# Kernel optimization log

Hardware: AMD Instinct MI355X
Metric: run time of the kernel (lower is better)

## Reference

```python
import jax, jax.numpy as jnp
import numpy as np

HIDDEN = 1024
FFN = 3584
N_EXPERTS = 8
TOP_K = 2


def setup_inputs() -> dict:
    key = jax.random.key(0)
    k1, k2, k3, k4 = jax.random.split(key, 4)
    B, S = 1, 1024
    hidden_states = jax.random.normal(k1, (B, S, HIDDEN), dtype=jnp.float32)
    gate_w = jax.random.normal(k2, (N_EXPERTS, HIDDEN), dtype=jnp.float32) * 0.02
    w_gate_up = jax.random.normal(k3, (N_EXPERTS, HIDDEN, 2 * FFN), dtype=jnp.float32) * 0.02
    w_down = jax.random.normal(k4, (N_EXPERTS, FFN, HIDDEN), dtype=jnp.float32) * 0.02
    return {"hidden_states": hidden_states, "gate_w": gate_w,
            "w_gate_up": w_gate_up, "w_down": w_down}


def reference(hidden_states, gate_w, w_gate_up, w_down):
    B, S, H = hidden_states.shape
    x = hidden_states.reshape(-1, H)                       # [T, H]
    T = x.shape[0]
    E = gate_w.shape[0]

    # Router
    router_logits = x @ gate_w.T                           # [T, E]
    probs = jax.nn.softmax(router_logits.astype(jnp.float32), axis=-1)
    routing_weights, selected = jax.lax.top_k(probs, TOP_K)  # [T, k]
    routing_weights = routing_weights / routing_weights.sum(-1, keepdims=True)

    # Dense combine matrix equivalent to permute->grouped GEMM->unpermute
    combine = jnp.zeros((T, E), probs.dtype).at[
        jnp.arange(T)[:, None], selected].add(routing_weights)  # [T, E]

    # Grouped SwiGLU expert MLPs (all experts over all tokens, masked by combine)
    gu = jnp.einsum('th,ehf->etf', x, w_gate_up)           # [E, T, 2F]
    Fdim = w_down.shape[1]
    gate_proj, up_proj = gu[..., :Fdim], gu[..., Fdim:]
    act = jax.nn.silu(gate_proj) * up_proj                 # [E, T, F]
    down = jnp.einsum('etf,efh->eth', act, w_down)         # [E, T, H]
    out = jnp.einsum('eth,te->th', down, combine.astype(down.dtype))
    return out.reshape(B, S, H), router_logits
```

## Files before the change

### kernel.cpp

```cpp
#include <hip/hip_runtime.h>
#include <hip/hip_bf16.h>
#include <math.h>

#define H 1024
#define F 3584
#define F2 7168
#define NE 8
#define T 1024

typedef __attribute__((ext_vector_type(4))) float f32x4;
typedef __attribute__((ext_vector_type(8))) short bf16x8;
typedef __attribute__((ext_vector_type(4))) unsigned u32x4;

__device__ inline short f2bf(float f) {
  union { float f; unsigned u; } v; v.f = f;
  unsigned r = (v.u + 0x7FFFu + ((v.u >> 16) & 1u)) >> 16;
  return (short)r;
}

__device__ inline unsigned pkbf(float a, float b) {
  unsigned r;
  asm("v_cvt_pk_bf16_f32 %0, %1, %2" : "=v"(r) : "v"(a), "v"(b));
  return r;
}

__device__ inline void gload16(const void* g, void* l) {
  __builtin_amdgcn_global_load_lds(
      (const __attribute__((address_space(1))) void*)g,
      (__attribute__((address_space(3))) void*)l, 16, 0, 0);
}

__global__ __launch_bounds__(64) void router_k(
    const float* __restrict__ x, const float* __restrict__ gw,
    float* __restrict__ logits, int* __restrict__ cnt,
    int* __restrict__ tok_e, int* __restrict__ tok_r, float* __restrict__ tok_w)
{
  int t = blockIdx.x, l = threadIdx.x;
  const float* xr = x + (size_t)t * H;
  double acc[NE];
  #pragma unroll
  for (int e = 0; e < NE; ++e) acc[e] = 0.0;
  for (int j = 0; j < H / 64; ++j) {
    int h = j * 64 + l;
    float xv = xr[h];
    #pragma unroll
    for (int e = 0; e < NE; ++e) acc[e] += (double)xv * (double)gw[e * H + h];
  }
  #pragma unroll
  for (int off = 32; off >= 1; off >>= 1) {
    #pragma unroll
    for (int e = 0; e < NE; ++e) acc[e] += __shfl_down(acc[e], off, 64);
  }
  if (l == 0) {
    float lg[NE];
    #pragma unroll
    for (int e = 0; e < NE; ++e) { lg[e] = (float)acc[e]; logits[t * NE + e] = lg[e]; }
    int i0 = 0;
    for (int e = 1; e < NE; ++e) if (lg[e] > lg[i0]) i0 = e;
    int i1 = (i0 == 0) ? 1 : 0;
    for (int e = 0; e < NE; ++e) if (e != i0 && lg[e] > lg[i1]) i1 = e;
    float w0 = 1.f / (1.f + expf(lg[i1] - lg[i0]));
    float w1 = 1.f / (1.f + expf(lg[i0] - lg[i1]));
    int r0 = atomicAdd(&cnt[i0], 1);
    int r1 = atomicAdd(&cnt[i1], 1);
    tok_e[2 * t] = i0;     tok_r[2 * t] = r0;     tok_w[2 * t] = w0;
    tok_e[2 * t + 1] = i1; tok_r[2 * t + 1] = r1; tok_w[2 * t + 1] = w1;
  }
}

__global__ __launch_bounds__(1024) void build_k(
    const int* __restrict__ cnt, int* __restrict__ base,
    const int* __restrict__ tok_e, const int* __restrict__ tok_r,
    const float* __restrict__ tok_w, int* __restrict__ gtok, float* __restrict__ gws)
{
  __shared__ int sb[NE];
  if (threadIdx.x == 0) {
    int s = 0;
    for (int e = 0; e < NE; ++e) { sb[e] = s; base[e] = s; s += cnt[e]; }
  }
  __syncthreads();
  int t = threadIdx.x;
  #pragma unroll
  for (int k = 0; k < 2; ++k) {
    int e = tok_e[2 * t + k];
    int slot = sb[e] + tok_r[2 * t + k];
    gtok[slot] = t;
    gws[slot] = tok_w[2 * t + k];
  }
}

__global__ __launch_bounds__(256, 4) void ffn1_k(
    const float* __restrict__ x, const float* __restrict__ wgu,
    const int* __restrict__ cnt, const int* __restrict__ base,
    const int* __restrict__ gtok, unsigned short* __restrict__ act)
{
  int wg = (blockIdx.x & 7) * 448 + (blockIdx.x >> 3);
  int mB = wg & 15;
  int rest = wg >> 4;
  int e = rest / 28, p = rest % 28;
  int n = cnt[e];
  int m0 = mB * 64;
  if (m0 >= n) return;
  int sb = base[e];
  int tid = threadIdx.x;
  int wv = tid >> 6, lane = tid & 63, lr = lane & 15, lg = lane >> 4;

  __shared__ __align__(16) float smem[10240];
  char* sBb = (char*)smem;
  char* sAb = (char*)(smem + 8192);

  int bchunk = lane ^ wv;
  int tc = bchunk * 4;
  int gc = (tc < 128) ? (p * 128 + tc) : (F + p * 128 + (tc - 128));
  const float* Bsrc = wgu + (size_t)e * H * F2 + (size_t)(wv * 8) * F2 + gc;

  int ar0 = wv * 16 + (lane >> 3);
  int ar1 = ar0 + 8;
  int as0 = (lane & 7) ^ (ar0 & 7);
  int as1 = (lane & 7) ^ (ar1 & 7);
  int sl0 = m0 + ar0; if (sl0 >= n) sl0 = n - 1;
  int sl1 = m0 + ar1; if (sl1 >= n) sl1 = n - 1;
  const float* Asrc0 = x + (size_t)gtok[sb + sl0] * H + as0 * 4;
  const float* Asrc1 = x + (size_t)gtok[sb + sl1] * H + as1 * 4;

  int rboff[4];
  #pragma unroll
  for (int cf = 0; cf < 4; ++cf) {
    int col = ((cf < 2) ? (wv * 32 + cf * 16) : (128 + wv * 32 + (cf - 2) * 16)) + lr;
    rboff[cf] = lg * 8 * 1024 + ((col * 4) ^ (lg << 4));
  }
  int raoff0[4], raoff1[4];
  #pragma unroll
  for (int mf = 0; mf < 4; ++mf) {
    int row = mf * 16 + lr;
    raoff0[mf] = row * 128 + ((((lg << 1) | 0) ^ (row & 7)) << 4);
    raoff1[mf] = row * 128 + ((((lg << 1) | 1) ^ (row & 7)) << 4);
  }

  f32x4 acc[4][4];
  #pragma unroll
  for (int mf = 0; mf < 4; ++mf)
    #pragma unroll
    for (int cf = 0; cf < 4; ++cf) acc[mf][cf] = (f32x4)0.f;

  for (int s = 0; s < 32; ++s) {
    const float* bs = Bsrc + (size_t)s * 32 * F2;
    #pragma unroll
    for (int j = 0; j < 8; ++j)
      gload16(bs + (size_t)j * F2, sBb + (wv * 8 + j) * 1024);
    gload16(Asrc0 + s * 32, sAb + (wv * 16) * 128);
    gload16(Asrc1 + s * 32, sAb + (wv * 16 + 8) * 128);
    asm volatile("s_waitcnt vmcnt(0)" ::: "memory");
    __builtin_amdgcn_s_barrier();
    asm volatile("" ::: "memory");

    bf16x8 bfr[4];
    #pragma unroll
    for (int cf = 0; cf < 4; ++cf) {
      float f0 = *(const float*)(sBb + rboff[cf]);
      float f1 = *(const float*)(sBb + rboff[cf] + 1024);
      float f2 = *(const float*)(sBb + rboff[cf] + 2048);
      float f3 = *(const float*)(sBb + rboff[cf] + 3072);
      float f4 = *(const float*)(sBb + rboff[cf] + 4096);
      float f5 = *(const float*)(sBb + rboff[cf] + 5120);
      float f6 = *(const float*)(sBb + rboff[cf] + 6144);
      float f7 = *(const float*)(sBb + rboff[cf] + 7168);
      union { u32x4 u; bf16x8 h; } cv;
      cv.u[0] = pkbf(f0, f1); cv.u[1] = pkbf(f2, f3);
      cv.u[2] = pkbf(f4, f5); cv.u[3] = pkbf(f6, f7);
      bfr[cf] = cv.h;
    }
    #pragma unroll
    for (int mf = 0; mf < 4; ++mf) {
      f32x4 a0 = *(const f32x4*)(sAb + raoff0[mf]);
      f32x4 a1 = *(const f32x4*)(sAb + raoff1[mf]);
      union { u32x4 u; bf16x8 h; } cv;
      cv.u[0] = pkbf(a0[0], a0[1]); cv.u[1] = pkbf(a0[2], a0[3]);
      cv.u[2] = pkbf(a1[0], a1[1]); cv.u[3] = pkbf(a1[2], a1[3]);
      bf16x8 af = cv.h;
      acc[mf][0] = __builtin_amdgcn_mfma_f32_16x16x32_bf16(af, bfr[0], acc[mf][0], 0, 0, 0);
      acc[mf][1] = __builtin_amdgcn_mfma_f32_16x16x32_bf16(af, bfr[1], acc[mf][1], 0, 0, 0);
      acc[mf][2] = __builtin_amdgcn_mfma_f32_16x16x32_bf16(af, bfr[2], acc[mf][2], 0, 0, 0);
      acc[mf][3] = __builtin_amdgcn_mfma_f32_16x16x32_bf16(af, bfr[3], acc[mf][3], 0, 0, 0);
    }
    asm volatile("s_waitcnt lgkmcnt(0)" ::: "memory");
    __builtin_amdgcn_s_barrier();
    asm volatile("" ::: "memory");
  }

  #pragma unroll
  for (int mf = 0; mf < 4; ++mf) {
    #pragma unroll
    for (int g = 0; g < 2; ++g) {
      int fcol = p * 128 + wv * 32 + g * 16 + lr;
      #pragma unroll
      for (int r = 0; r < 4; ++r) {
        int sl = m0 + mf * 16 + lg * 4 + r;
        if (sl < n) {
          float gg = acc[mf][g][r], u = acc[mf][g + 2][r];
          act[(size_t)(sb + sl) * F + fcol] = (unsigned short)f2bf(gg / (1.f + expf(-gg)) * u);
        }
      }
    }
  }
}

__global__ __launch_bounds__(256, 4) void ffn2_k(
    const unsigned short* __restrict__ act, const float* __restrict__ wd,
    const int* __restrict__ cnt, const int* __restrict__ base,
    const int* __restrict__ gtok, const float* __restrict__ gws,
    float* __restrict__ out)
{
  int wg = (blockIdx.x & 7) * 512 + (blockIdx.x >> 3);
  int mB = wg & 15;
  int rest = wg >> 4;
  int p = rest & 7;
  int kh = (rest >> 3) & 3;
  int e = rest >> 5;
  int n = cnt[e];
  int m0 = mB * 64;
  if (m0 >= n) return;
  int sb = base[e];
  int tid = threadIdx.x;
  int wv = tid >> 6, lane = tid & 63, lr = lane & 15, lg = lane >> 4;
  const int kbase = kh * 896;

  __shared__ __align__(16) char smem2[20480];
  char* sBb = smem2;
  char* sAb = smem2 + 16384;

  int bchunk = (lane & 31) ^ wv;
  const float* Bsrc = wd + (size_t)e * F * H
                    + (size_t)(kbase + wv * 8 + (lane >> 5)) * H + p * 128 + bchunk * 4;

  int arow = wv * 16 + (lane >> 2);
  int aseg = (lane & 3) ^ (arow & 3);
  int asl = m0 + arow; if (asl >= n) asl = n - 1;
  const unsigned short* Asrc = act + (size_t)(sb + asl) * F + kbase + aseg * 8;

  int rboff[2];
  #pragma unroll
  for (int cf = 0; cf < 2; ++cf) {
    int col = wv * 32 + cf * 16 + lr;
    rboff[cf] = lg * 8 * 512 + ((col * 4) ^ (lg << 4));
  }
  int raoff[4];
  #pragma unroll
  for (int mf = 0; mf < 4; ++mf) {
    int row = mf * 16 + lr;
    raoff[mf] = row * 64 + ((lg ^ (row & 3)) << 4);
  }

  f32x4 acc[4][2];
  #pragma unroll
  for (int mf = 0; mf < 4; ++mf) { acc[mf][0] = (f32x4)0.f; acc[mf][1] = (f32x4)0.f; }

  for (int s = 0; s < 28; ++s) {
    const float* bs = Bsrc + (size_t)s * 32 * H;
    #pragma unroll
    for (int j = 0; j < 4; ++j)
      gload16(bs + (size_t)(2 * j) * H, sBb + (wv * 8 + 2 * j) * 512);
    gload16(Asrc + s * 32, sAb + wv * 16 * 64);
    asm volatile("s_waitcnt vmcnt(0)" ::: "memory");
    __builtin_amdgcn_s_barrier();
    asm volatile("" ::: "memory");

    bf16x8 bfr[2];
    #pragma unroll
    for (int cf = 0; cf < 2; ++cf) {
      float f0 = *(const float*)(sBb + rboff[cf]);
      float f1 = *(const float*)(sBb + rboff[cf] + 512);
      float f2 = *(const float*)(sBb + rboff[cf] + 1024);
      float f3 = *(const float*)(sBb + rboff[cf] + 1536);
      float f4 = *(const float*)(sBb + rboff[cf] + 2048);
      float f5 = *(const float*)(sBb + rboff[cf] + 2560);
      float f6 = *(const float*)(sBb + rboff[cf] + 3072);
      float f7 = *(const float*)(sBb + rboff[cf] + 3584);
      union { u32x4 u; bf16x8 h; } cv;
      cv.u[0] = pkbf(f0, f1); cv.u[1] = pkbf(f2, f3);
      cv.u[2] = pkbf(f4, f5); cv.u[3] = pkbf(f6, f7);
      bfr[cf] = cv.h;
    }
    #pragma unroll
    for (int mf = 0; mf < 4; ++mf) {
      bf16x8 af = *(const bf16x8*)(sAb + raoff[mf]);
      acc[mf][0] = __builtin_amdgcn_mfma_f32_16x16x32_bf16(af, bfr[0], acc[mf][0], 0, 0, 0);
      acc[mf][1] = __builtin_amdgcn_mfma_f32_16x16x32_bf16(af, bfr[1], acc[mf][1], 0, 0, 0);
    }
    asm volatile("s_waitcnt lgkmcnt(0)" ::: "memory");
    __builtin_amdgcn_s_barrier();
    asm volatile("" ::: "memory");
  }

  #pragma unroll
  for (int mf = 0; mf < 4; ++mf) {
    #pragma unroll
    for (int cf = 0; cf < 2; ++cf) {
      int col = p * 128 + wv * 32 + cf * 16 + lr;
      #pragma unroll
      for (int r = 0; r < 4; ++r) {
        int sl = m0 + mf * 16 + lg * 4 + r;
        if (sl < n) {
          int slot = sb + sl;
          atomicAdd(&out[(size_t)gtok[slot] * H + col], gws[slot] * acc[mf][cf][r]);
        }
      }
    }
  }
}

extern "C" void kernel_launch(void* const* d_in, const int* in_sizes, int n_in,
                              void* d_out, int out_size, void* d_ws, size_t ws_size,
                              hipStream_t stream)
{
  const float* x   = (const float*)d_in[0];
  const float* gw  = (const float*)d_in[1];
  const float* wgu = (const float*)d_in[2];
  const float* wdn = (const float*)d_in[3];
  float* out = (float*)d_out;
  float* logits = out + (size_t)T * H;

  char* w = (char*)d_ws;
  int*   cnt = (int*)(w);
  int*   bs  = (int*)(w + 32);
  int*   te  = (int*)(w + 64);
  int*   tr  = (int*)(w + 64 + 8192);
  float* tw  = (float*)(w + 64 + 16384);
  int*   gt  = (int*)(w + 64 + 24576);
  float* gwt = (float*)(w + 64 + 32768);
  unsigned short* act = (unsigned short*)(w + 65536);

  hipMemsetAsync(d_out, 0, (size_t)T * H * sizeof(float), stream);
  hipMemsetAsync(cnt, 0, NE * sizeof(int), stream);
  router_k<<<T, 64, 0, stream>>>(x, gw, logits, cnt, te, tr, tw);
  build_k<<<1, 1024, 0, stream>>>(cnt, bs, te, tr, tw, gt, gwt);
  ffn1_k<<<3584, 256, 0, stream>>>(x, wgu, cnt, bs, gt, act);
  ffn2_k<<<4096, 256, 0, stream>>>(act, wdn, cnt, bs, gt, gwt, out);
}
```

Baseline: 277.3 us.

## Double-buffer LDS tiles in both expert FFN kernels to overlap loads with MFMA

Both grouped GEMM kernels now keep two LDS buffers and issue the next K-step's direct-to-LDS global loads before computing on the current one. A partial vmcnt wait lets the next step's loads stay in flight during compute. This targets the exposed global-memory latency caused by the old issue-wait-compute loop. It doubles LDS use (ffn1 to 80 KB) and lowers ffn1's occupancy hint from 4 to 2 blocks per CU, which reduces latency hiding across blocks.

```diff
diff --git a/kernel.cpp b/kernel.cpp
--- a/kernel.cpp
+++ b/kernel.cpp
@@ -89,7 +89,7 @@
   }
 }
 
-__global__ __launch_bounds__(256, 4) void ffn1_k(
+__global__ __launch_bounds__(256, 2) void ffn1_k(
     const float* __restrict__ x, const float* __restrict__ wgu,
     const int* __restrict__ cnt, const int* __restrict__ base,
     const int* __restrict__ gtok, unsigned short* __restrict__ act)
@@ -105,9 +105,11 @@
   int tid = threadIdx.x;
   int wv = tid >> 6, lane = tid & 63, lr = lane & 15, lg = lane >> 4;
 
-  __shared__ __align__(16) float smem[10240];
-  char* sBb = (char*)smem;
-  char* sAb = (char*)(smem + 8192);
+  __shared__ __align__(16) char smem[81920];
+  char* sB0 = smem;
+  char* sA0 = smem + 32768;
+  char* sB1 = smem + 40960;
+  char* sA1 = smem + 73728;
 
   int bchunk = lane ^ wv;
   int tc = bchunk * 4;
@@ -143,28 +145,40 @@
     #pragma unroll
     for (int cf = 0; cf < 4; ++cf) acc[mf][cf] = (f32x4)0.f;
 
+#define ISSUE1(S, bB, bA) { \
+    const float* bs_ = Bsrc + (size_t)(S) * 32 * F2; \
+    _Pragma("unroll") for (int j = 0; j < 8; ++j) \
+      gload16(bs_ + (size_t)j * F2, (bB) + (wv * 8 + j) * 1024); \
+    gload16(Asrc0 + (S) * 32, (bA) + (wv * 16) * 128); \
+    gload16(Asrc1 + (S) * 32, (bA) + (wv * 16 + 8) * 128); }
+
+  ISSUE1(0, sB0, sA0);
+
   for (int s = 0; s < 32; ++s) {
-    const float* bs = Bsrc + (size_t)s * 32 * F2;
-    #pragma unroll
-    for (int j = 0; j < 8; ++j)
-      gload16(bs + (size_t)j * F2, sBb + (wv * 8 + j) * 1024);
-    gload16(Asrc0 + s * 32, sAb + (wv * 16) * 128);
-    gload16(Asrc1 + s * 32, sAb + (wv * 16 + 8) * 128);
-    asm volatile("s_waitcnt vmcnt(0)" ::: "memory");
+    char* cB = (s & 1) ? sB1 : sB0;
+    char* cA = (s & 1) ? sA1 : sA0;
+    char* nB = (s & 1) ? sB0 : sB1;
+    char* nA = (s & 1) ? sA0 : sA1;
+    if (s + 1 < 32) {
+      ISSUE1(s + 1, nB, nA);
+      asm volatile("s_waitcnt vmcnt(10)" ::: "memory");
+    } else {
+      asm volatile("s_waitcnt vmcnt(0)" ::: "memory");
+    }
     __builtin_amdgcn_s_barrier();
     asm volatile("" ::: "memory");
 
     bf16x8 bfr[4];
     #pragma unroll
     for (int cf = 0; cf < 4; ++cf) {
-      float f0 = *(const float*)(sBb + rboff[cf]);
-      float f1 = *(const float*)(sBb + rboff[cf] + 1024);
-      float f2 = *(const float*)(sBb + rboff[cf] + 2048);
-      float f3 = *(const float*)(sBb + rboff[cf] + 3072);
-      float f4 = *(const float*)(sBb + rboff[cf] + 4096);
-      float f5 = *(const float*)(sBb + rboff[cf] + 5120);
-      float f6 = *(const float*)(sBb + rboff[cf] + 6144);
-      float f7 = *(const float*)(sBb + rboff[cf] + 7168);
+      float f0 = *(const float*)(cB + rboff[cf]);
+      float f1 = *(const float*)(cB + rboff[cf] + 1024);
+      float f2 = *(const float*)(cB + rboff[cf] + 2048);
+      float f3 = *(const float*)(cB + rboff[cf] + 3072);
+      float f4 = *(const float*)(cB + rboff[cf] + 4096);
+      float f5 = *(const float*)(cB + rboff[cf] + 5120);
+      float f6 = *(const float*)(cB + rboff[cf] + 6144);
+      float f7 = *(const float*)(cB + rboff[cf] + 7168);
       union { u32x4 u; bf16x8 h; } cv;
       cv.u[0] = pkbf(f0, f1); cv.u[1] = pkbf(f2, f3);
       cv.u[2] = pkbf(f4, f5); cv.u[3] = pkbf(f6, f7);
@@ -172,8 +186,8 @@
     }
     #pragma unroll
     for (int mf = 0; mf < 4; ++mf) {
-      f32x4 a0 = *(const f32x4*)(sAb + raoff0[mf]);
-      f32x4 a1 = *(const f32x4*)(sAb + raoff1[mf]);
+      f32x4 a0 = *(const f32x4*)(cA + raoff0[mf]);
+      f32x4 a1 = *(const f32x4*)(cA + raoff1[mf]);
       union { u32x4 u; bf16x8 h; } cv;
       cv.u[0] = pkbf(a0[0], a0[1]); cv.u[1] = pkbf(a0[2], a0[3]);
       cv.u[2] = pkbf(a1[0], a1[1]); cv.u[3] = pkbf(a1[2], a1[3]);
@@ -187,6 +201,7 @@
     __builtin_amdgcn_s_barrier();
     asm volatile("" ::: "memory");
   }
+#undef ISSUE1
 
   #pragma unroll
   for (int mf = 0; mf < 4; ++mf) {
@@ -225,9 +240,11 @@
   int wv = tid >> 6, lane = tid & 63, lr = lane & 15, lg = lane >> 4;
   const int kbase = kh * 896;
 
-  __shared__ __align__(16) char smem2[20480];
-  char* sBb = smem2;
-  char* sAb = smem2 + 16384;
+  __shared__ __align__(16) char smem2[40960];
+  char* sB0 = smem2;
+  char* sA0 = smem2 + 16384;
+  char* sB1 = smem2 + 20480;
+  char* sA1 = smem2 + 36864;
 
   int bchunk = (lane & 31) ^ wv;
   const float* Bsrc = wd + (size_t)e * F * H
@@ -255,27 +272,39 @@
   #pragma unroll
   for (int mf = 0; mf < 4; ++mf) { acc[mf][0] = (f32x4)0.f; acc[mf][1] = (f32x4)0.f; }
 
+#define ISSUE2(S, bB, bA) { \
+    const float* bs_ = Bsrc + (size_t)(S) * 32 * H; \
+    _Pragma("unroll") for (int j = 0; j < 4; ++j) \
+      gload16(bs_ + (size_t)(2 * j) * H, (bB) + (wv * 8 + 2 * j) * 512); \
+    gload16(Asrc + (S) * 32, (bA) + wv * 16 * 64); }
+
+  ISSUE2(0, sB0, sA0);
+
   for (int s = 0; s < 28; ++s) {
-    const float* bs = Bsrc + (size_t)s * 32 * H;
-    #pragma unroll
-    for (int j = 0; j < 4; ++j)
-      gload16(bs + (size_t)(2 * j) * H, sBb + (wv * 8 + 2 * j) * 512);
-    gload16(Asrc + s * 32, sAb + wv * 16 * 64);
-    asm volatile("s_waitcnt vmcnt(0)" ::: "memory");
+    char* cB = (s & 1) ? sB1 : sB0;
+    char* cA = (s & 1) ? sA1 : sA0;
+    char* nB = (s & 1) ? sB0 : sB1;
+    char* nA = (s & 1) ? sA0 : sA1;
+    if (s + 1 < 28) {
+      ISSUE2(s + 1, nB, nA);
+      asm volatile("s_waitcnt vmcnt(5)" ::: "memory");
+    } else {
+      asm volatile("s_waitcnt vmcnt(0)" ::: "memory");
+    }
     __builtin_amdgcn_s_barrier();
     asm volatile("" ::: "memory");
 
     bf16x8 bfr[2];
     #pragma unroll
     for (int cf = 0; cf < 2; ++cf) {
-      float f0 = *(const float*)(sBb + rboff[cf]);
-      float f1 = *(const float*)(sBb + rboff[cf] + 512);
-      float f2 = *(const float*)(sBb + rboff[cf] + 1024);
-      float f3 = *(const float*)(sBb + rboff[cf] + 1536);
-      float f4 = *(const float*)(sBb + rboff[cf] + 2048);
-      float f5 = *(const float*)(sBb + rboff[cf] + 2560);
-      float f6 = *(const float*)(sBb + rboff[cf] + 3072);
-      float f7 = *(const float*)(sBb + rboff[cf] + 3584);
+      float f0 = *(const float*)(cB + rboff[cf]);
+      float f1 = *(const float*)(cB + rboff[cf] + 512);
+      float f2 = *(const float*)(cB + rboff[cf] + 1024);
+      float f3 = *(const float*)(cB + rboff[cf] + 1536);
+      float f4 = *(const float*)(cB + rboff[cf] + 2048);
+      float f5 = *(const float*)(cB + rboff[cf] + 2560);
+      float f6 = *(const float*)(cB + rboff[cf] + 3072);
+      float f7 = *(const float*)(cB + rboff[cf] + 3584);
       union { u32x4 u; bf16x8 h; } cv;
       cv.u[0] = pkbf(f0, f1); cv.u[1] = pkbf(f2, f3);
       cv.u[2] = pkbf(f4, f5); cv.u[3] = pkbf(f6, f7);
@@ -283,7 +312,7 @@
     }
     #pragma unroll
     for (int mf = 0; mf < 4; ++mf) {
-      bf16x8 af = *(const bf16x8*)(sAb + raoff[mf]);
+      bf16x8 af = *(const bf16x8*)(cA + raoff[mf]);
       acc[mf][0] = __builtin_amdgcn_mfma_f32_16x16x32_bf16(af, bfr[0], acc[mf][0], 0, 0, 0);
       acc[mf][1] = __builtin_amdgcn_mfma_f32_16x16x32_bf16(af, bfr[1], acc[mf][1], 0, 0, 0);
     }
@@ -291,6 +320,7 @@
     __builtin_amdgcn_s_barrier();
     asm volatile("" ::: "memory");
   }
+#undef ISSUE2
 
   #pragma unroll
   for (int mf = 0; mf < 4; ++mf) {
```

Measured after the change: 276.2 us. Within noise of the previous version (-0.4%).
